# Optimization experiments

Measured on AMD Instinct MI355X. Metric: run time of the kernel, lower is better.

## Reference

```python
import jax, jax.numpy as jnp
import numpy as np

D_MODEL = 1024
NUM_HEADS = 16
D_K = D_MODEL // NUM_HEADS
B, S = 4, 2048


def setup_inputs() -> dict:
    key = jax.random.key(0)
    ks = jax.random.split(key, 11)
    s = 1.0 / np.sqrt(D_MODEL)  # torch Linear default init scale (uniform bound)
    def lin(k):
        kw, kb = jax.random.split(k)
        W = jax.random.uniform(kw, (D_MODEL, D_MODEL), jnp.float32, -s, s)
        b = jax.random.uniform(kb, (D_MODEL,), jnp.float32, -s, s)
        return W, b
    Wq, bq = lin(ks[0])
    Wk, bk = lin(ks[1])
    Wv, bv = lin(ks[2])
    Wo, bo = lin(ks[3])
    query = jax.random.normal(ks[4], (B, S, D_MODEL), jnp.float32)
    key_t = jax.random.normal(ks[5], (B, S, D_MODEL), jnp.float32)
    value = jax.random.normal(ks[6], (B, S, D_MODEL), jnp.float32)
    mask = jnp.ones((B, 1, 1, S), jnp.int32)
    return {"query": query, "key": key_t, "value": value, "mask": mask,
            "Wq": Wq, "bq": bq, "Wk": Wk, "bk": bk, "Wv": Wv, "bv": bv,
            "Wo": Wo, "bo": bo}


def _split_heads(x):
    # (B, S, D) -> (B, H, S, d_k)
    b, s, _ = x.shape
    return x.reshape(b, s, NUM_HEADS, D_K).transpose(0, 2, 1, 3)


def _mha(query, key, value, mask, Wq, bq, Wk, bk, Wv, bv, Wo, bo):
    Q = _split_heads(query @ Wq.T + bq)
    K = _split_heads(key @ Wk.T + bk)
    V = _split_heads(value @ Wv.T + bv)
    scores = jnp.einsum('bhqd,bhkd->bhqk', Q, K) / np.sqrt(D_K)
    scores = jnp.where(mask == 0, jnp.float32(-1e9), scores)
    attn = jax.nn.softmax(scores, axis=-1)
    out = jnp.einsum('bhqk,bhkd->bhqd', attn, V)  # (B,H,S,d_k)
    out = out.transpose(0, 2, 1, 3).reshape(out.shape[0], out.shape[2], D_MODEL)
    return out @ Wo.T + bo


def reference(query, key, value, mask, Wq, bq, Wk, bk, Wv, bv, Wo, bo):
    return _mha(query, key, value, mask, Wq, bq, Wk, bk, Wv, bv, Wo, bo)
```

## Files before the change

kernel.cpp:

```cpp
#include <hip/hip_runtime.h>


typedef unsigned short u16;
typedef __attribute__((ext_vector_type(8))) short short8;
typedef __attribute__((ext_vector_type(4))) float f32x4;

__device__ __forceinline__ u16 f2bf(float f) {
  union { float f; unsigned int u; } v; v.f = f;
  return (u16)((v.u + 0x7FFFu + ((v.u >> 16) & 1u)) >> 16);
}

__device__ __forceinline__ void gll16(const void* gptr, void* lptr) {
  __builtin_amdgcn_global_load_lds(
      (const __attribute__((address_space(1))) unsigned int*)gptr,
      (__attribute__((address_space(3))) unsigned int*)lptr, 16, 0, 0);
}

__device__ __forceinline__ void cvt8(const float* __restrict__ s,
                                     u16* __restrict__ d) {
  f32x4 a = *(const f32x4*)(s);
  f32x4 b = *(const f32x4*)(s + 4);
  short8 r;
  r[0] = (short)f2bf(a[0]); r[1] = (short)f2bf(a[1]);
  r[2] = (short)f2bf(a[2]); r[3] = (short)f2bf(a[3]);
  r[4] = (short)f2bf(b[0]); r[5] = (short)f2bf(b[1]);
  r[6] = (short)f2bf(b[2]); r[7] = (short)f2bf(b[3]);
  *(short8*)(d) = r;
}

__global__ void cvt_x(const float* __restrict__ s, u16* __restrict__ d, int n) {
  const int i = (blockIdx.x * 256 + threadIdx.x) * 8;
  if (i >= n) return;
  cvt8(s + i, d + i);
}

__global__ void cvt_w4(const float* __restrict__ w0, const float* __restrict__ w1,
                       const float* __restrict__ w2, const float* __restrict__ w3,
                       u16* __restrict__ d) {
  const int z = blockIdx.y;
  const float* s = (z == 0) ? w0 : (z == 1) ? w1 : (z == 2) ? w2 : w3;
  const int i = (blockIdx.x * 256 + threadIdx.x) * 8;
  cvt8(s + i, d + (size_t)z * 1048576 + i);
}

__global__ void cvt_all(const float* __restrict__ q, const float* __restrict__ k,
                        const float* __restrict__ v, const float* __restrict__ w0,
                        const float* __restrict__ w1, const float* __restrict__ w2,
                        const float* __restrict__ w3, u16* __restrict__ dx,
                        u16* __restrict__ dw) {
  const int z = blockIdx.y;
  if (z < 3) {
    const float* s = (z == 0) ? q : (z == 1) ? k : v;
    const int i = (blockIdx.x * 256 + threadIdx.x) * 8;
    cvt8(s + i, dx + (size_t)z * 8388608 + i);
  } else {
    const int bi = blockIdx.x;
    if (bi >= 2048) return;
    const int w = bi >> 9;
    const float* s = (w == 0) ? w0 : (w == 1) ? w1 : (w == 2) ? w2 : w3;
    const int i = ((bi & 511) * 256 + threadIdx.x) * 8;
    cvt8(s + i, dw + (size_t)w * 1048576 + i);
  }
}

__device__ __forceinline__ void xcd_swz(unsigned& bx, unsigned& by) {
  const unsigned nx = gridDim.x, nwg = nx * gridDim.y;
  if ((nwg & 7u) == 0u) {
    const unsigned lin = bx + nx * by;
    const unsigned swz = (lin & 7u) * (nwg >> 3) + (lin >> 3);
    bx = swz % nx;
    by = swz / nx;
  }
}

#define GM 128
#define GN 128
#define GK 32

template <typename TC, bool TRANS>
__global__ __launch_bounds__(256, 3) void gemm_bb(
    const u16* __restrict__ A, const u16* __restrict__ W,
    const float* __restrict__ bias, TC* __restrict__ C,
    int M, int N, int K, float scale)
{
  __shared__ __align__(16) u16 As[2][GM * GK];
  __shared__ __align__(16) u16 Bs[2][GN * GK];

  const int tid  = threadIdx.x;
  const int lane = tid & 63;
  const int l15  = lane & 15;
  const int quad = lane >> 4;
  const int wave = tid >> 6;
  unsigned bxu = blockIdx.x, byu = blockIdx.y;
  xcd_swz(bxu, byu);
  const int bm = byu * GM;
  const int bn = bxu * GN;
  const int wm = (wave >> 1) * 64;
  const int wn = (wave & 1) * 64;

  const f32x4 zero4 = {0.f, 0.f, 0.f, 0.f};
  f32x4 acc[4][4];
#pragma unroll
  for (int i = 0; i < 4; i++)
#pragma unroll
    for (int j = 0; j < 4; j++) acc[i][j] = zero4;

  const int srow = tid >> 2;
  const int chl  = (tid & 3) ^ ((tid >> 3) & 3);
  const u16* Ag = A + (size_t)(bm + srow) * K + chl * 8;
  const u16* Wg = W + (size_t)(bn + srow) * K + chl * 8;
  const size_t rowskip = (size_t)64 * K;
  const int chpA = quad ^ ((l15 >> 1) & 3);

  gll16(Ag, &As[0][tid * 8]);
  gll16(Ag + rowskip, &As[0][tid * 8 + 2048]);
  gll16(Wg, &Bs[0][tid * 8]);
  gll16(Wg + rowskip, &Bs[0][tid * 8 + 2048]);

  int buf = 0;
  for (int k0 = 0; k0 < K; k0 += GK) {
    __syncthreads();
    if (k0 + GK < K) {
      const int nb = buf ^ 1;
      gll16(Ag + k0 + GK, &As[nb][tid * 8]);
      gll16(Ag + k0 + GK + rowskip, &As[nb][tid * 8 + 2048]);
      gll16(Wg + k0 + GK, &Bs[nb][tid * 8]);
      gll16(Wg + k0 + GK + rowskip, &Bs[nb][tid * 8 + 2048]);
    }

    short8 af[4], bfr[4];
#pragma unroll
    for (int mi = 0; mi < 4; mi++)
      af[mi] = *(const short8*)&As[buf][(wm + mi * 16 + l15) * GK + chpA * 8];
#pragma unroll
    for (int ni = 0; ni < 4; ni++)
      bfr[ni] = *(const short8*)&Bs[buf][(wn + ni * 16 + l15) * GK + chpA * 8];
#pragma unroll
    for (int mi = 0; mi < 4; mi++)
#pragma unroll
      for (int ni = 0; ni < 4; ni++)
        acc[mi][ni] = __builtin_amdgcn_mfma_f32_16x16x32_bf16(
            af[mi], bfr[ni], acc[mi][ni], 0, 0, 0);
    buf ^= 1;
  }

  float bval[4];
#pragma unroll
  for (int ni = 0; ni < 4; ni++) bval[ni] = bias[bn + wn + ni * 16 + l15];
#pragma unroll
  for (int mi = 0; mi < 4; mi++) {
    const int m0 = bm + wm + mi * 16 + quad * 4;
#pragma unroll
    for (int ni = 0; ni < 4; ni++) {
      const int n = bn + wn + ni * 16 + l15;
      if constexpr (TRANS) {
        ushort4 w;
        w.x = f2bf((acc[mi][ni][0] + bval[ni]) * scale);
        w.y = f2bf((acc[mi][ni][1] + bval[ni]) * scale);
        w.z = f2bf((acc[mi][ni][2] + bval[ni]) * scale);
        w.w = f2bf((acc[mi][ni][3] + bval[ni]) * scale);
        *(ushort4*)((u16*)C + (size_t)n * M + m0) = w;
      } else {
#pragma unroll
        for (int r = 0; r < 4; r++) {
          const float v = (acc[mi][ni][r] + bval[ni]) * scale;
          if constexpr (sizeof(TC) == 2)
            C[(size_t)(m0 + r) * N + n] = f2bf(v);
          else
            C[(size_t)(m0 + r) * N + n] = v;
        }
      }
    }
  }
}

__global__ __launch_bounds__(256, 3) void gemm_qkv(
    const u16* __restrict__ Ab, const u16* __restrict__ Wc,
    const float* __restrict__ bq, const float* __restrict__ bk,
    const float* __restrict__ bv, u16* __restrict__ Qo,
    u16* __restrict__ Ko, u16* __restrict__ Vo, float qscale)
{
  const int M = 8192, N = 1024, K = 1024;
  const int z = blockIdx.z;
  const u16* A = Ab + (size_t)z * 8388608;
  const u16* W = Wc + (size_t)z * 1048576;
  const float* bias = (z == 0) ? bq : (z == 1) ? bk : bv;
  u16* C = (z == 0) ? Qo : (z == 1) ? Ko : Vo;
  const float scale = (z == 0) ? qscale : 1.0f;
  const bool trans = (z == 2);

  __shared__ __align__(16) u16 As[2][GM * GK];
  __shared__ __align__(16) u16 Bs[2][GN * GK];

  const int tid  = threadIdx.x;
  const int lane = tid & 63;
  const int l15  = lane & 15;
  const int quad = lane >> 4;
  const int wave = tid >> 6;
  unsigned bxu = blockIdx.x, byu = blockIdx.y;
  xcd_swz(bxu, byu);
  const int bm = byu * GM;
  const int bn = bxu * GN;
  const int wm = (wave >> 1) * 64;
  const int wn = (wave & 1) * 64;

  const f32x4 zero4 = {0.f, 0.f, 0.f, 0.f};
  f32x4 acc[4][4];
#pragma unroll
  for (int i = 0; i < 4; i++)
#pragma unroll
    for (int j = 0; j < 4; j++) acc[i][j] = zero4;

  const int srow = tid >> 2;
  const int chl  = (tid & 3) ^ ((tid >> 3) & 3);
  const u16* Ag = A + (size_t)(bm + srow) * K + chl * 8;
  const u16* Wg = W + (size_t)(bn + srow) * K + chl * 8;
  const size_t rowskip = (size_t)64 * K;
  const int chpA = quad ^ ((l15 >> 1) & 3);

  gll16(Ag, &As[0][tid * 8]);
  gll16(Ag + rowskip, &As[0][tid * 8 + 2048]);
  gll16(Wg, &Bs[0][tid * 8]);
  gll16(Wg + rowskip, &Bs[0][tid * 8 + 2048]);

  int buf = 0;
  for (int k0 = 0; k0 < K; k0 += GK) {
    __syncthreads();
    if (k0 + GK < K) {
      const int nb = buf ^ 1;
      gll16(Ag + k0 + GK, &As[nb][tid * 8]);
      gll16(Ag + k0 + GK + rowskip, &As[nb][tid * 8 + 2048]);
      gll16(Wg + k0 + GK, &Bs[nb][tid * 8]);
      gll16(Wg + k0 + GK + rowskip, &Bs[nb][tid * 8 + 2048]);
    }

    short8 af[4], bfr[4];
#pragma unroll
    for (int mi = 0; mi < 4; mi++)
      af[mi] = *(const short8*)&As[buf][(wm + mi * 16 + l15) * GK + chpA * 8];
#pragma unroll
    for (int ni = 0; ni < 4; ni++)
      bfr[ni] = *(const short8*)&Bs[buf][(wn + ni * 16 + l15) * GK + chpA * 8];
#pragma unroll
    for (int mi = 0; mi < 4; mi++)
#pragma unroll
      for (int ni = 0; ni < 4; ni++)
        acc[mi][ni] = __builtin_amdgcn_mfma_f32_16x16x32_bf16(
            af[mi], bfr[ni], acc[mi][ni], 0, 0, 0);
    buf ^= 1;
  }

  float bval[4];
#pragma unroll
  for (int ni = 0; ni < 4; ni++) bval[ni] = bias[bn + wn + ni * 16 + l15];
#pragma unroll
  for (int mi = 0; mi < 4; mi++) {
    const int m0 = bm + wm + mi * 16 + quad * 4;
#pragma unroll
    for (int ni = 0; ni < 4; ni++) {
      const int n = bn + wn + ni * 16 + l15;
      if (trans) {
        ushort4 w;
        w.x = f2bf(acc[mi][ni][0] + bval[ni]);
        w.y = f2bf(acc[mi][ni][1] + bval[ni]);
        w.z = f2bf(acc[mi][ni][2] + bval[ni]);
        w.w = f2bf(acc[mi][ni][3] + bval[ni]);
        *(ushort4*)(C + (size_t)n * M + m0) = w;
      } else {
#pragma unroll
        for (int r = 0; r < 4; r++)
          C[(size_t)(m0 + r) * N + n] = f2bf((acc[mi][ni][r] + bval[ni]) * scale);
      }
    }
  }
}

__global__ __launch_bounds__(256, 4) void attn_fused(
    const u16* __restrict__ Qb, const u16* __restrict__ Kb,
    const u16* __restrict__ VtG, const int* __restrict__ mask,
    u16* __restrict__ Ob)
{
  constexpr int S = 2048, D = 1024;
  __shared__ __align__(16) u16 Ks[64 * 64];
  __shared__ __align__(16) u16 Vs[64 * 64];
  __shared__ __align__(16) u16 Pt[4][32 * 64];

  const int tid  = threadIdx.x;
  const int lane = tid & 63;
  const int wave = tid >> 6;
  const int l15  = lane & 15;
  const int quad = lane >> 4;

  const int lin = blockIdx.x + 16 * blockIdx.y;
  const int swz = (lin & 7) * 128 + (lin >> 3);
  const int b  = swz >> 8;
  const int h  = (swz >> 4) & 15;
  const int qw = (swz & 15) * 128 + wave * 32;

  const u16* Qp = Qb + (size_t)b * S * D + h * 64;
  const u16* Kp = Kb + (size_t)b * S * D + h * 64;
  const u16* Vg = VtG + (size_t)h * 64 * 8192 + b * 2048;
  const int* mp = mask + b * S;

  short8 qf[2][2];
#pragma unroll
  for (int qb = 0; qb < 2; qb++)
#pragma unroll
    for (int c = 0; c < 2; c++)
      qf[qb][c] = *(const short8*)&Qp[(size_t)(qw + qb * 16 + l15) * D + c * 32 + quad * 8];

  const f32x4 zero4 = {0.f, 0.f, 0.f, 0.f};
  f32x4 o_acc[2][4];
#pragma unroll
  for (int qb = 0; qb < 2; qb++)
#pragma unroll
    for (int ni = 0; ni < 4; ni++) o_acc[qb][ni] = zero4;
  f32x4 l_acc[2] = {zero4, zero4};

  const short8 one8 = {(short)0x3f80, (short)0x3f80, (short)0x3f80, (short)0x3f80,
                       (short)0x3f80, (short)0x3f80, (short)0x3f80, (short)0x3f80};

  const int srow = tid >> 3;
  const int chl  = (tid & 7) ^ (srow & 7);
  const int fsw  = l15 & 7;

  unsigned int* tbs = (unsigned int*)&Pt[0][0];
  {
    const int t8 = tid * 8;
    int4 a  = *(const int4*)&mp[t8];
    int4 c4 = *(const int4*)&mp[t8 + 4];
    int ok = ((a.x & a.y & a.z & a.w & c4.x & c4.y & c4.z & c4.w) != 0);
    unsigned long long bb = __ballot(ok);
    if (lane == 0) {
      unsigned int byt = 0;
#pragma unroll
      for (int g = 0; g < 8; g++)
        if (((bb >> (8 * g)) & 0xffull) == 0xffull) byt |= 1u << g;
      tbs[wave] = byt;
    }
  }

#pragma unroll
  for (int p = 0; p < 2; p++)
    gll16(Kp + (size_t)(p * 32 + srow) * D + chl * 8, &Ks[p * 2048 + tid * 8]);

  __syncthreads();
  const unsigned int tilebits = __builtin_amdgcn_readfirstlane(
      tbs[0] | (tbs[1] << 8) | (tbs[2] << 16) | (tbs[3] << 24));

  for (int kt = 0; kt < S; kt += 64) {
    __syncthreads();

#pragma unroll
    for (int p = 0; p < 2; p++)
      gll16(Vg + (size_t)(p * 32 + srow) * 8192 + kt + chl * 8,
            &Vs[p * 2048 + tid * 8]);

    f32x4 sc[2][4];
#pragma unroll
    for (int qb = 0; qb < 2; qb++)
#pragma unroll
      for (int s = 0; s < 4; s++) sc[qb][s] = zero4;
    __builtin_amdgcn_s_setprio(1);
#pragma unroll
    for (int c = 0; c < 2; c++)
#pragma unroll
      for (int s = 0; s < 4; s++) {
        short8 kf = *(const short8*)
            &Ks[(s * 16 + l15) * 64 + ((c * 4 + quad) ^ fsw) * 8];
        sc[0][s] = __builtin_amdgcn_mfma_f32_16x16x32_bf16(kf, qf[0][c], sc[0][s], 0, 0, 0);
        sc[1][s] = __builtin_amdgcn_mfma_f32_16x16x32_bf16(kf, qf[1][c], sc[1][s], 0, 0, 0);
      }
    __builtin_amdgcn_s_setprio(0);

    const bool open = (tilebits >> (kt >> 6)) & 1;
    if (open) {
#pragma unroll
      for (int qb = 0; qb < 2; qb++) {
        const int qrow = qb * 16 + l15;
#pragma unroll
        for (int s = 0; s < 4; s++) {
          unsigned int t[4];
#pragma unroll
          for (int r = 0; r < 4; r++) {
            union { float f; unsigned int u; } pu;
            pu.f = __builtin_amdgcn_exp2f(sc[qb][s][r]);
            t[r] = pu.u;
          }
          uint2 w;
          w.x = __builtin_amdgcn_perm(t[1], t[0], 0x07060302u);
          w.y = __builtin_amdgcn_perm(t[3], t[2], 0x07060302u);
          const int phys = (s * 2 + (quad >> 1)) ^ fsw;
          *(uint2*)&Pt[wave][qrow * 64 + phys * 8 + (quad & 1) * 4] = w;
        }
      }
    } else {
      f32x4 cm[4];
#pragma unroll
      for (int s = 0; s < 4; s++) {
        int4 mv = *(const int4*)&mp[kt + s * 16 + quad * 4];
        cm[s][0] = mv.x ? 0.f : -1.0e9f;
        cm[s][1] = mv.y ? 0.f : -1.0e9f;
        cm[s][2] = mv.z ? 0.f : -1.0e9f;
        cm[s][3] = mv.w ? 0.f : -1.0e9f;
      }
#pragma unroll
      for (int qb = 0; qb < 2; qb++) {
        const int qrow = qb * 16 + l15;
#pragma unroll
        for (int s = 0; s < 4; s++) {
          unsigned int t[4];
#pragma unroll
          for (int r = 0; r < 4; r++) {
            union { float f; unsigned int u; } pu;
            pu.f = __builtin_amdgcn_exp2f(sc[qb][s][r] + cm[s][r]);
            t[r] = pu.u;
          }
          uint2 w;
          w.x = __builtin_amdgcn_perm(t[1], t[0], 0x07060302u);
          w.y = __builtin_amdgcn_perm(t[3], t[2], 0x07060302u);
          const int phys = (s * 2 + (quad >> 1)) ^ fsw;
          *(uint2*)&Pt[wave][qrow * 64 + phys * 8 + (quad & 1) * 4] = w;
        }
      }
    }

    __syncthreads();

    if (kt + 64 < S) {
#pragma unroll
      for (int p = 0; p < 2; p++)
        gll16(Kp + (size_t)(kt + 64 + p * 32 + srow) * D + chl * 8,
              &Ks[p * 2048 + tid * 8]);
    }

    __builtin_amdgcn_s_setprio(1);
#pragma unroll
    for (int c = 0; c < 2; c++) {
      short8 pf[2];
#pragma unroll
      for (int qb = 0; qb < 2; qb++)
        pf[qb] = *(const short8*)
            &Pt[wave][(qb * 16 + l15) * 64 + ((c * 4 + quad) ^ fsw) * 8];
      l_acc[0] = __builtin_amdgcn_mfma_f32_16x16x32_bf16(pf[0], one8, l_acc[0], 0, 0, 0);
      l_acc[1] = __builtin_amdgcn_mfma_f32_16x16x32_bf16(pf[1], one8, l_acc[1], 0, 0, 0);
#pragma unroll
      for (int ni = 0; ni < 4; ni++) {
        short8 vf = *(const short8*)
            &Vs[(ni * 16 + l15) * 64 + ((c * 4 + quad) ^ fsw) * 8];
        o_acc[0][ni] = __builtin_amdgcn_mfma_f32_16x16x32_bf16(pf[0], vf, o_acc[0][ni], 0, 0, 0);
        o_acc[1][ni] = __builtin_amdgcn_mfma_f32_16x16x32_bf16(pf[1], vf, o_acc[1][ni], 0, 0, 0);
      }
    }
    __builtin_amdgcn_s_setprio(0);
  }

  float rl[2][4];
#pragma unroll
  for (int qb = 0; qb < 2; qb++)
#pragma unroll
    for (int r = 0; r < 4; r++) rl[qb][r] = 1.0f / l_acc[qb][r];
#pragma unroll
  for (int qb = 0; qb < 2; qb++) {
    const int q0 = qw + qb * 16 + quad * 4;
#pragma unroll
    for (int ni = 0; ni < 4; ni++)
#pragma unroll
      for (int r = 0; r < 4; r++)
        Ob[(size_t)(b * S + q0 + r) * D + h * 64 + ni * 16 + l15] =
            f2bf(o_acc[qb][ni][r] * rl[qb][r]);
  }
}

extern "C" void kernel_launch(void* const* d_in, const int* in_sizes, int n_in,
                              void* d_out, int out_size, void* d_ws, size_t ws_size,
                              hipStream_t stream) {
  const int M = 8192, N = 1024, K = 1024;
  const float* q    = (const float*)d_in[0];
  const float* k    = (const float*)d_in[1];
  const float* v    = (const float*)d_in[2];
  const int*   mask = (const int*)d_in[3];
  const float* Wq = (const float*)d_in[4];
  const float* bq = (const float*)d_in[5];
  const float* Wk = (const float*)d_in[6];
  const float* bk = (const float*)d_in[7];
  const float* Wv = (const float*)d_in[8];
  const float* bv = (const float*)d_in[9];
  const float* Wo = (const float*)d_in[10];
  const float* bo = (const float*)d_in[11];

  const size_t MN = (size_t)M * N;
  const float QSC = 0.125f * 1.44269504f;

  dim3 bb(256);
  dim3 gg(N / GN, M / GM);

  const size_t need_batched = (6 * MN + 4 * 1048576) * sizeof(u16);
  if (ws_size >= need_batched) {
    u16* Ax  = (u16*)d_ws;
    u16* Qb  = Ax + 3 * MN;
    u16* Kb  = Ax + 4 * MN;
    u16* VtG = Ax + 5 * MN;
    u16* Wc  = Ax + 6 * MN;
    u16* Ob  = Ax;

    cvt_all<<<dim3(4096, 4), bb, 0, stream>>>(q, k, v, Wq, Wk, Wv, Wo, Ax, Wc);
    gemm_qkv<<<dim3(8, 64, 3), bb, 0, stream>>>(Ax, Wc, bq, bk, bv, Qb, Kb, VtG, QSC);
    attn_fused<<<dim3(16, 64), bb, 0, stream>>>(Qb, Kb, VtG, mask, Ob);
    gemm_bb<float, false><<<gg, bb, 0, stream>>>(Ob, Wc + 3 * 1048576, bo,
                                                 (float*)d_out, M, N, K, 1.0f);
  } else {
    u16* Qb  = (u16*)d_ws;
    u16* Kb  = Qb + MN;
    u16* VtG = Kb + MN;
    u16* Ob  = VtG + MN;
    u16* Wc  = Ob + MN;
    const int xblk = (int)(MN / (256 * 8));

    cvt_w4<<<dim3(512, 4), bb, 0, stream>>>(Wq, Wk, Wv, Wo, Wc);

    cvt_x<<<xblk, bb, 0, stream>>>(q, Ob, M * N);
    gemm_bb<u16, false><<<gg, bb, 0, stream>>>(Ob, Wc + 0 * 1048576, bq, Qb, M, N, K, QSC);
    cvt_x<<<xblk, bb, 0, stream>>>(k, Ob, M * N);
    gemm_bb<u16, false><<<gg, bb, 0, stream>>>(Ob, Wc + 1 * 1048576, bk, Kb, M, N, K, 1.0f);
    cvt_x<<<xblk, bb, 0, stream>>>(v, Ob, M * N);
    gemm_bb<u16, true><<<gg, bb, 0, stream>>>(Ob, Wc + 2 * 1048576, bv, VtG, M, N, K, 1.0f);

    attn_fused<<<dim3(16, 64), bb, 0, stream>>>(Qb, Kb, VtG, mask, Ob);

    gemm_bb<float, false><<<gg, bb, 0, stream>>>(Ob, Wc + 3 * 1048576, bo,
                                                 (float*)d_out, M, N, K, 1.0f);
  }
}
```

Measured before the change: 336.8 us.

## Enlarge QKV GEMM tile to 256x128 with 512 threads and split conversion kernels

Replaces the fused QKV projection GEMM with a version using 256x128 output tiles and 8 waves per block, so each loaded W tile is reused across twice as many rows and the grid has half as many blocks. The combined fp32-to-bf16 conversion kernel is split back into separate weight and activation conversion launches. This raises shared memory per block and changes occupancy, and it adds one kernel launch.

```diff
diff --git a/kernel.cpp b/kernel.cpp
--- a/kernel.cpp
+++ b/kernel.cpp
@@ -34,6 +34,14 @@
   cvt8(s + i, d + i);
 }
 
+__global__ void cvt_x3(const float* __restrict__ q, const float* __restrict__ k,
+                       const float* __restrict__ v, u16* __restrict__ d) {
+  const int z = blockIdx.y;
+  const float* s = (z == 0) ? q : (z == 1) ? k : v;
+  const int i = (blockIdx.x * 256 + threadIdx.x) * 8;
+  cvt8(s + i, d + (size_t)z * 8388608 + i);
+}
+
 __global__ void cvt_w4(const float* __restrict__ w0, const float* __restrict__ w1,
                        const float* __restrict__ w2, const float* __restrict__ w3,
                        u16* __restrict__ d) {
@@ -41,26 +49,6 @@
   const float* s = (z == 0) ? w0 : (z == 1) ? w1 : (z == 2) ? w2 : w3;
   const int i = (blockIdx.x * 256 + threadIdx.x) * 8;
   cvt8(s + i, d + (size_t)z * 1048576 + i);
-}
-
-__global__ void cvt_all(const float* __restrict__ q, const float* __restrict__ k,
-                        const float* __restrict__ v, const float* __restrict__ w0,
-                        const float* __restrict__ w1, const float* __restrict__ w2,
-                        const float* __restrict__ w3, u16* __restrict__ dx,
-                        u16* __restrict__ dw) {
-  const int z = blockIdx.y;
-  if (z < 3) {
-    const float* s = (z == 0) ? q : (z == 1) ? k : v;
-    const int i = (blockIdx.x * 256 + threadIdx.x) * 8;
-    cvt8(s + i, dx + (size_t)z * 8388608 + i);
-  } else {
-    const int bi = blockIdx.x;
-    if (bi >= 2048) return;
-    const int w = bi >> 9;
-    const float* s = (w == 0) ? w0 : (w == 1) ? w1 : (w == 2) ? w2 : w3;
-    const int i = ((bi & 511) * 256 + threadIdx.x) * 8;
-    cvt8(s + i, dw + (size_t)w * 1048576 + i);
-  }
 }
 
 __device__ __forceinline__ void xcd_swz(unsigned& bx, unsigned& by) {
@@ -174,7 +162,10 @@
   }
 }
 
-__global__ __launch_bounds__(256, 3) void gemm_qkv(
+#define HM 256
+#define HN 128
+
+__global__ __launch_bounds__(512, 4) void gemm_qkv2(
     const u16* __restrict__ Ab, const u16* __restrict__ Wc,
     const float* __restrict__ bq, const float* __restrict__ bk,
     const float* __restrict__ bv, u16* __restrict__ Qo,
@@ -189,8 +180,8 @@
   const float scale = (z == 0) ? qscale : 1.0f;
   const bool trans = (z == 2);
 
-  __shared__ __align__(16) u16 As[2][GM * GK];
-  __shared__ __align__(16) u16 Bs[2][GN * GK];
+  __shared__ __align__(16) u16 As[2][HM * GK];
+  __shared__ __align__(16) u16 Bs[2][HN * GK];
 
   const int tid  = threadIdx.x;
   const int lane = tid & 63;
@@ -199,8 +190,8 @@
   const int wave = tid >> 6;
   unsigned bxu = blockIdx.x, byu = blockIdx.y;
   xcd_swz(bxu, byu);
-  const int bm = byu * GM;
-  const int bn = bxu * GN;
+  const int bm = byu * HM;
+  const int bn = bxu * HN;
   const int wm = (wave >> 1) * 64;
   const int wn = (wave & 1) * 64;
 
@@ -215,13 +206,12 @@
   const int chl  = (tid & 3) ^ ((tid >> 3) & 3);
   const u16* Ag = A + (size_t)(bm + srow) * K + chl * 8;
   const u16* Wg = W + (size_t)(bn + srow) * K + chl * 8;
-  const size_t rowskip = (size_t)64 * K;
+  const size_t rowskipA = (size_t)128 * K;
   const int chpA = quad ^ ((l15 >> 1) & 3);
 
   gll16(Ag, &As[0][tid * 8]);
-  gll16(Ag + rowskip, &As[0][tid * 8 + 2048]);
+  gll16(Ag + rowskipA, &As[0][tid * 8 + 4096]);
   gll16(Wg, &Bs[0][tid * 8]);
-  gll16(Wg + rowskip, &Bs[0][tid * 8 + 2048]);
 
   int buf = 0;
   for (int k0 = 0; k0 < K; k0 += GK) {
@@ -229,9 +219,8 @@
     if (k0 + GK < K) {
       const int nb = buf ^ 1;
       gll16(Ag + k0 + GK, &As[nb][tid * 8]);
-      gll16(Ag + k0 + GK + rowskip, &As[nb][tid * 8 + 2048]);
+      gll16(Ag + k0 + GK + rowskipA, &As[nb][tid * 8 + 4096]);
       gll16(Wg + k0 + GK, &Bs[nb][tid * 8]);
-      gll16(Wg + k0 + GK + rowskip, &Bs[nb][tid * 8 + 2048]);
     }
 
     short8 af[4], bfr[4];
@@ -504,8 +493,10 @@
     u16* Wc  = Ax + 6 * MN;
     u16* Ob  = Ax;
 
-    cvt_all<<<dim3(4096, 4), bb, 0, stream>>>(q, k, v, Wq, Wk, Wv, Wo, Ax, Wc);
-    gemm_qkv<<<dim3(8, 64, 3), bb, 0, stream>>>(Ax, Wc, bq, bk, bv, Qb, Kb, VtG, QSC);
+    cvt_w4<<<dim3(512, 4), bb, 0, stream>>>(Wq, Wk, Wv, Wo, Wc);
+    cvt_x3<<<dim3(4096, 3), bb, 0, stream>>>(q, k, v, Ax);
+    gemm_qkv2<<<dim3(N / HN, M / HM, 3), dim3(512), 0, stream>>>(
+        Ax, Wc, bq, bk, bv, Qb, Kb, VtG, QSC);
     attn_fused<<<dim3(16, 64), bb, 0, stream>>>(Qb, Kb, VtG, mask, Ob);
     gemm_bb<float, false><<<gg, bb, 0, stream>>>(Ob, Wc + 3 * 1048576, bo,
                                                  (float*)d_out, M, N, K, 1.0f);
```

After: 334.3 us. Within noise of the previous version (-0.7%).
